# Kernel tuning notes

Measured on AMD Instinct MI355X. Metric: run time of the kernel, lower is better.

Reference implementation:

```python
import jax, jax.numpy as jnp
import numpy as np

K = 16            # neighbors
QUERY_CHUNK = 256 # SE is applied per chunk of this many query points (matches torch loop)
EPS = 1e-5        # BatchNorm eps (eval mode, running stats)


def bn(x, g, b, m, v):
    # eval-mode batchnorm over last axis (channel-last layout here)
    return (x - m) * (g / jnp.sqrt(v + EPS)) + b


def setup_inputs() -> dict:
    key = jax.random.key(0)
    ks = jax.random.split(key, 16)
    B, Cin, N = 4, 128, 4096
    H, Cout = 128, 256
    se_h = Cout // 4
    r = lambda k, s, sc=1.0: jax.random.normal(k, s, jnp.float32) * sc
    return dict(
        x=r(ks[0], (B, Cin, N)),
        W_edge=r(ks[1], (H, 2 * Cin), 0.05),          # edge_mlp conv2d 1x1
        bn1_g=jnp.ones((H,), jnp.float32), bn1_b=jnp.zeros((H,), jnp.float32),
        bn1_m=r(ks[2], (H,), 0.1), bn1_v=jax.random.uniform(ks[3], (H,), jnp.float32) + 0.5,
        w_att=r(ks[4], (H,), 0.1),                     # att_conv (1,H,1,1)
        W_fuse=r(ks[5], (Cout, H), 0.05),              # fuse conv1d
        bn2_g=jnp.ones((Cout,), jnp.float32), bn2_b=jnp.zeros((Cout,), jnp.float32),
        bn2_m=r(ks[6], (Cout,), 0.1), bn2_v=jax.random.uniform(ks[7], (Cout,), jnp.float32) + 0.5,
        fc1_w=r(ks[8], (se_h, Cout), 0.05), fc1_b=jnp.zeros((se_h,), jnp.float32),
        fc2_w=r(ks[9], (Cout, se_h), 0.05), fc2_b=jnp.zeros((Cout,), jnp.float32),
        W_res=r(ks[10], (Cout, Cin), 0.05),            # res_conv conv1d (in!=out)
        bn3_g=jnp.ones((Cout,), jnp.float32), bn3_b=jnp.zeros((Cout,), jnp.float32),
        bn3_m=r(ks[11], (Cout,), 0.1), bn3_v=jax.random.uniform(ks[12], (Cout,), jnp.float32) + 0.5,
    )


def reference(x, W_edge, bn1_g, bn1_b, bn1_m, bn1_v, w_att,
              W_fuse, bn2_g, bn2_b, bn2_m, bn2_v,
              fc1_w, fc1_b, fc2_w, fc2_b,
              W_res, bn3_g, bn3_b, bn3_m, bn3_v):
    B, Cin, N = x.shape
    x_t = jnp.swapaxes(x, 1, 2)  # (B,N,Cin)

    # KNN on features (dynamic=False -> knn on x.transpose); squared euclidean
    # has the same ordering as torch.cdist(p=2).
    sq = jnp.sum(x_t * x_t, axis=-1)                               # (B,N)
    d2 = sq[:, :, None] + sq[:, None, :] - 2.0 * jnp.einsum('bnc,bmc->bnm', x_t, x_t)
    _, idx = jax.lax.top_k(-d2, K)                                  # (B,N,K) smallest dists

    neigh = jax.vmap(lambda p, i: p[i])(x_t, idx)                   # (B,N,K,Cin)
    center = jnp.broadcast_to(x_t[:, :, None, :], neigh.shape)      # (B,N,K,Cin)
    edge = jnp.concatenate([neigh - center, center], axis=-1)       # (B,N,K,2Cin)

    # edge_mlp: 1x1 conv + BN + ReLU
    h = jax.nn.relu(bn(jnp.einsum('bnkc,hc->bnkh', edge, W_edge),
                       bn1_g, bn1_b, bn1_m, bn1_v))                 # (B,N,K,H)

    # attention over neighbors
    att = jax.nn.softmax(jnp.einsum('bnkh,h->bnk', h, w_att), axis=-1)
    agg = jnp.einsum('bnkh,bnk->bnh', h, att)                       # (B,N,H)

    # fuse conv1d + BN + ReLU
    out = jax.nn.relu(bn(jnp.einsum('bnh,oh->bno', agg, W_fuse),
                         bn2_g, bn2_b, bn2_m, bn2_v))               # (B,N,Cout)

    # SE channel attention, applied per query chunk (matches torch loop semantics)
    Cout = out.shape[-1]
    nc = N // QUERY_CHUNK
    oc = out.reshape(B, nc, QUERY_CHUNK, Cout)
    s = oc.mean(axis=2)                                             # (B,nc,Cout)
    s = jax.nn.relu(jnp.einsum('bmc,hc->bmh', s, fc1_w) + fc1_b)
    s = jax.nn.sigmoid(jnp.einsum('bmh,ch->bmc', s, fc2_w) + fc2_b)
    out = (oc * s[:, :, None, :]).reshape(B, N, Cout)

    # residual projection (in_channels != out_channels)
    res = bn(jnp.einsum('bnc,oc->bno', x_t, W_res), bn3_g, bn3_b, bn3_m, bn3_v)
    out = out + res
    return jnp.swapaxes(out, 1, 2)                                  # (B,Cout,N)
```

## Files before the change

kernel.cpp:

```cpp
#include <hip/hip_runtime.h>
#include <cstddef>

typedef __bf16 bf16;
typedef __bf16 bf16x8 __attribute__((ext_vector_type(8)));
typedef float  f32x4  __attribute__((ext_vector_type(4)));
typedef unsigned short u16;
typedef unsigned long long u64;

#define MFMA16x16(a, b, c) __builtin_amdgcn_mfma_f32_16x16x32_bf16((a), (b), (c), 0, 0, 0)

namespace {
constexpr int BB   = 4;
constexpr int CIN  = 128;
constexpr int NPT  = 4096;
constexpr int KNBR = 16;
constexpr int HED  = 128;
constexpr int COUT = 256;
}

__device__ __forceinline__ double mk_keyd(float d, unsigned mlo ) {
  const u64 k = ((u64)__float_as_uint(d) << 32) | mlo;
  return __longlong_as_double((long long)k);
}
__device__ __forceinline__ int key_idx(double kd) {
  return (int)((__double_as_longlong(kd) >> 20) & 0xFFF);
}

__device__ __forceinline__ void sort16d(double* k) {
  #pragma unroll
  for (int sz = 2; sz <= 16; sz <<= 1) {
    #pragma unroll
    for (int st = sz >> 1; st > 0; st >>= 1) {
      #pragma unroll
      for (int i = 0; i < 16; ++i) {
        const int j = i ^ st;
        if (j > i) {
          const bool up = ((i & sz) == 0);
          const double a = k[i], c = k[j];
          const double lo = fmin(a, c), hi = fmax(a, c);
          k[i] = up ? lo : hi;
          k[j] = up ? hi : lo;
        }
      }
    }
  }
}

__device__ __forceinline__ void merge16d(double* R, const double* B) {
  double t[16];
  #pragma unroll
  for (int i = 0; i < 16; ++i) t[i] = fmin(R[i], B[15 - i]);
  #pragma unroll
  for (int st = 8; st > 0; st >>= 1) {
    #pragma unroll
    for (int i = 0; i < 16; ++i) {
      const int j = i ^ st;
      if (j > i) {
        const double a = t[i], c = t[j];
        t[i] = fmin(a, c);
        t[j] = fmax(a, c);
      }
    }
  }
  #pragma unroll
  for (int i = 0; i < 16; ++i) R[i] = t[i];
}

__device__ __forceinline__ void shfl_merge16d(double* R, int mask) {
  double B[16];
  #pragma unroll
  for (int i = 0; i < 16; ++i) B[i] = __shfl_xor(R[i], mask, 64);
  merge16d(R, B);
}

__global__ __launch_bounds__(256) void k_prepw(const float* __restrict__ x,
                                               bf16* __restrict__ xh,
                                               bf16* __restrict__ xl,
                                               float* __restrict__ sq,
                                               const float* __restrict__ We,
                                               const float* __restrict__ Wf,
                                               const float* __restrict__ Wr,
                                               bf16* __restrict__ Web,
                                               bf16* __restrict__ Wfb,
                                               bf16* __restrict__ Wrb,
                                               float* __restrict__ partp) {
  __shared__ __attribute__((aligned(16))) bf16 th[64][136];
  __shared__ __attribute__((aligned(16))) bf16 tl[64][136];
  __shared__ float sqp[4][64];
  const int blk = blockIdx.x;
  const int tid = threadIdx.x;
  if (blk >= 256) {
    if (blk < 640) {
      const int i = (blk - 256) * 256 + tid;
      const int a = i >> 15;
      const int j = i & 32767;
      const float* src = (a == 0) ? We : (a == 1) ? Wf : Wr;
      bf16*        dst = (a == 0) ? Web : (a == 1) ? Wfb : Wrb;
      dst[j] = (bf16)src[j];
    } else {
      for (int i = tid; i < 64 * COUT; i += 256) partp[i] = 0.f;
    }
    return;
  }
  const int b   = blk >> 6;
  const int n0  = (blk & 63) << 6;
  const int nl  = tid & 63;
  const int cg  = tid >> 6;
  const float* xb = x + (size_t)b * CIN * NPT;
  float acc = 0.f;
  #pragma unroll
  for (int rep = 0; rep < 32; ++rep) {
    const int c = rep * 4 + cg;
    const float v = xb[(size_t)c * NPT + n0 + nl];
    const bf16 h = (bf16)v;
    const bf16 l = (bf16)(v - (float)h);
    acc += v * v;
    th[nl][c] = h;
    tl[nl][c] = l;
  }
  sqp[cg][nl] = acc;
  __syncthreads();
  bf16* xho = xh + ((size_t)b * NPT + n0) * CIN;
  bf16* xlo = xl + ((size_t)b * NPT + n0) * CIN;
  #pragma unroll
  for (int rep = 0; rep < 32; ++rep) {
    const int e = rep * 256 + tid;
    const int r = e >> 7;
    const int c = e & 127;
    xho[(size_t)r * CIN + c] = th[r][c];
    xlo[(size_t)r * CIN + c] = tl[r][c];
  }
  if (tid < 64) {
    sq[b * NPT + n0 + tid] = sqp[0][tid] + sqp[1][tid] + sqp[2][tid] + sqp[3][tid];
  }
}

__global__ __launch_bounds__(256, 2) void k_knn(const bf16* __restrict__ xh,
                                                const bf16* __restrict__ xl,
                                                const float* __restrict__ sq,
                                                int* __restrict__ knn_idx) {
  __shared__ double Lk[32][66];
  const int tid  = threadIdx.x;
  const int w    = tid >> 6;
  const int lane = tid & 63;
  const int col  = lane & 15;
  const int quad = lane >> 4;
  const int bid  = blockIdx.x;
  const int swz  = ((bid & 7) << 6) | (bid >> 3);
  const int b    = swz >> 7;
  const int q0   = (swz & 127) << 5;
  const bf16*  xhb = xh + (size_t)b * NPT * CIN;
  const bf16*  xlb = xl + (size_t)b * NPT * CIN;
  const float* sqb = sq + b * NPT;

  bf16x8 qh[2][4], ql[2][4];
  float sqn[2];
  #pragma unroll
  for (int t = 0; t < 2; ++t) {
    const bf16* qrh = xhb + (size_t)(q0 + t * 16 + col) * CIN + quad * 8;
    const bf16* qrl = xlb + (size_t)(q0 + t * 16 + col) * CIN + quad * 8;
    #pragma unroll
    for (int ks = 0; ks < 4; ++ks) {
      qh[t][ks] = *(const bf16x8*)(qrh + ks * 32);
      ql[t][ks] = *(const bf16x8*)(qrl + ks * 32);
    }
    sqn[t] = sqb[q0 + t * 16 + col];
  }

  const double INF = __builtin_inf();
  double R0[16], R1[16];
  #pragma unroll
  for (int i = 0; i < 16; ++i) { R0[i] = INF; R1[i] = INF; }

  const int cbase = w << 10;
  for (int mt = 0; mt < 16; ++mt) {
    const int m0 = cbase + (mt << 6);
    double k0[16], k1[16];
    #pragma unroll
    for (int cb = 0; cb < 4; ++cb) {
      const bf16* crh = xhb + (size_t)(m0 + cb * 16 + col) * CIN + quad * 8;
      const bf16* crl = xlb + (size_t)(m0 + cb * 16 + col) * CIN + quad * 8;
      f32x4 a0 = {0.f, 0.f, 0.f, 0.f};
      f32x4 a1 = {0.f, 0.f, 0.f, 0.f};
      #pragma unroll
      for (int ks = 0; ks < 4; ++ks) {
        const bf16x8 ch_ = *(const bf16x8*)(crh + ks * 32);
        const bf16x8 cl_ = *(const bf16x8*)(crl + ks * 32);
        a0 = MFMA16x16(cl_, qh[0][ks], a0);
        a0 = MFMA16x16(ch_, ql[0][ks], a0);
        a0 = MFMA16x16(ch_, qh[0][ks], a0);
        a1 = MFMA16x16(cl_, qh[1][ks], a1);
        a1 = MFMA16x16(ch_, ql[1][ks], a1);
        a1 = MFMA16x16(ch_, qh[1][ks], a1);
      }
      const f32x4 sqm = *(const f32x4*)(sqb + m0 + cb * 16 + quad * 4);
      const unsigned mlo0 = (unsigned)(m0 + cb * 16 + quad * 4) << 20;
      #pragma unroll
      for (int r = 0; r < 4; ++r) {
        k0[cb * 4 + r] = mk_keyd((sqn[0] + sqm[r]) - 2.0f * a0[r], mlo0 + ((unsigned)r << 20));
        k1[cb * 4 + r] = mk_keyd((sqn[1] + sqm[r]) - 2.0f * a1[r], mlo0 + ((unsigned)r << 20));
      }
    }
    sort16d(k0); merge16d(R0, k0);
    sort16d(k1); merge16d(R1, k1);
  }

  shfl_merge16d(R0, 16);
  shfl_merge16d(R0, 32);
  shfl_merge16d(R1, 16);
  shfl_merge16d(R1, 32);

  if (quad == 0) {
    #pragma unroll
    for (int i = 0; i < 16; ++i) {
      Lk[col][w * 16 + i]        = R0[i];
      Lk[16 | col][w * 16 + i]   = R1[i];
    }
  }
  __syncthreads();

  if (tid < 64) {
    const int q = tid >> 1;
    const int j = tid & 1;
    double A[16], Bv[16];
    #pragma unroll
    for (int i = 0; i < 16; ++i) {
      A[i]  = Lk[q][(2 * j) * 16 + i];
      Bv[i] = Lk[q][(2 * j + 1) * 16 + i];
    }
    merge16d(A, Bv);
    #pragma unroll
    for (int i = 0; i < 16; ++i) Lk[q][j * 16 + i] = A[i];
  }
  __syncthreads();
  if (tid < 32) {
    double A[16], Bv[16];
    #pragma unroll
    for (int i = 0; i < 16; ++i) {
      A[i]  = Lk[tid][i];
      Bv[i] = Lk[tid][16 + i];
    }
    merge16d(A, Bv);
    int* op = knn_idx + (size_t)(b * NPT + q0 + tid) * KNBR;
    #pragma unroll
    for (int i = 0; i < 16; ++i) op[i] = key_idx(A[i]);
  }
}

__global__ __launch_bounds__(256) void k_edge(const bf16* __restrict__ xh,
                                              const bf16* __restrict__ xl,
                                              const int* __restrict__ knn_idx,
                                              const bf16* __restrict__ We,
                                              const float* __restrict__ g1, const float* __restrict__ b1,
                                              const float* __restrict__ m1, const float* __restrict__ v1,
                                              const float* __restrict__ watt,
                                              bf16* __restrict__ agg) {
  __shared__ __attribute__((aligned(16))) bf16 Ew[4][16][264];
  __shared__ float s1[HED], t1[HED], wat[HED];
  const int tid  = threadIdx.x;
  const int w    = tid >> 6;
  const int lane = tid & 63;
  const int col  = lane & 15;
  const int quad = lane >> 4;
  if (tid < HED) {
    const float ss = g1[tid] / sqrtf(v1[tid] + 1e-5f);
    s1[tid] = ss;
    t1[tid] = b1[tid] - m1[tid] * ss;
    wat[tid] = watt[tid];
  }
  __syncthreads();
  const int bid = blockIdx.x;
  const int swz = ((bid & 7) << 7) | (bid >> 3);
  const int gw  = swz * 4 + w;
  for (int it = 0; it < 4; ++it) {
    const int p = gw * 4 + it;
    const int b = p >> 12;
    const int n = p & 4095;
    const bf16* xhb = xh + (size_t)b * NPT * CIN;
    const bf16* xlb = xl + (size_t)b * NPT * CIN;
    const int my = knn_idx[(size_t)p * KNBR + col];
    const int m  = __shfl(my, lane >> 2);
    const int sub = lane & 3;
    const int kn  = lane >> 2;
    const bf16* nh = xhb + (size_t)m * CIN + sub * 32;
    const bf16* nl_ = xlb + (size_t)m * CIN + sub * 32;
    const bf16* ch = xhb + (size_t)n * CIN + sub * 32;
    const bf16* cl = xlb + (size_t)n * CIN + sub * 32;
    #pragma unroll
    for (int j = 0; j < 4; ++j) {
      const bf16x8 nhv = *(const bf16x8*)(nh + j * 8);
      const bf16x8 nlv = *(const bf16x8*)(nl_ + j * 8);
      const bf16x8 chv = *(const bf16x8*)(ch + j * 8);
      const bf16x8 clv = *(const bf16x8*)(cl + j * 8);
      bf16x8 dv, cv;
      #pragma unroll
      for (int e = 0; e < 8; ++e) {
        const float nf = (float)nhv[e] + (float)nlv[e];
        const float cf = (float)chv[e] + (float)clv[e];
        dv[e] = (bf16)(nf - cf);
        cv[e] = (bf16)cf;
      }
      *(bf16x8*)&Ew[w][kn][sub * 32 + j * 8]       = dv;
      *(bf16x8*)&Ew[w][kn][128 + sub * 32 + j * 8] = cv;
    }
    const f32x4 zero4 = {0.f, 0.f, 0.f, 0.f};
    f32x4 acc[8];
    #pragma unroll
    for (int hb = 0; hb < 8; ++hb) acc[hb] = zero4;
    #pragma unroll
    for (int ks = 0; ks < 8; ++ks) {
      const bf16x8 af = *(const bf16x8*)&Ew[w][col][ks * 32 + quad * 8];
      #pragma unroll
      for (int hb = 0; hb < 8; ++hb) {
        const bf16x8 bfv = *(const bf16x8*)(We + (size_t)(hb * 16 + col) * 256 + ks * 32 + quad * 8);
        acc[hb] = MFMA16x16(af, bfv, acc[hb]);
      }
    }
    float h[8][4];
    float lg[4] = {0.f, 0.f, 0.f, 0.f};
    #pragma unroll
    for (int hb = 0; hb < 8; ++hb) {
      const int hc = hb * 16 + col;
      const float ss = s1[hc], tt = t1[hc], ww = wat[hc];
      #pragma unroll
      for (int r = 0; r < 4; ++r) {
        const float hv = fmaxf(acc[hb][r] * ss + tt, 0.f);
        h[hb][r] = hv;
        lg[r] += hv * ww;
      }
    }
    #pragma unroll
    for (int r = 0; r < 4; ++r) {
      float vv = lg[r];
      vv += __shfl_xor(vv, 1);
      vv += __shfl_xor(vv, 2);
      vv += __shfl_xor(vv, 4);
      vv += __shfl_xor(vv, 8);
      lg[r] = vv;
    }
    float mx = fmaxf(fmaxf(lg[0], lg[1]), fmaxf(lg[2], lg[3]));
    mx = fmaxf(mx, __shfl_xor(mx, 16));
    mx = fmaxf(mx, __shfl_xor(mx, 32));
    float ex[4];
    float sm = 0.f;
    #pragma unroll
    for (int r = 0; r < 4; ++r) { ex[r] = expf(lg[r] - mx); sm += ex[r]; }
    sm += __shfl_xor(sm, 16);
    sm += __shfl_xor(sm, 32);
    const float inv = 1.0f / sm;
    float ag[8];
    #pragma unroll
    for (int hb = 0; hb < 8; ++hb) {
      float a = h[hb][0] * ex[0] + h[hb][1] * ex[1] + h[hb][2] * ex[2] + h[hb][3] * ex[3];
      a += __shfl_xor(a, 16);
      a += __shfl_xor(a, 32);
      ag[hb] = a * inv;
    }
    if (quad == 0) {
      bf16* ao = agg + (size_t)p * HED;
      #pragma unroll
      for (int hb = 0; hb < 8; ++hb) ao[hb * 16 + col] = (bf16)ag[hb];
    }
  }
}

__global__ __launch_bounds__(256) void k_fuse(const bf16* __restrict__ agg,
                                              const bf16* __restrict__ Wf,
                                              const float* __restrict__ g2, const float* __restrict__ b2,
                                              const float* __restrict__ m2, const float* __restrict__ v2,
                                              bf16* __restrict__ outp,
                                              float* __restrict__ partp) {
  const int tid  = threadIdx.x;
  const int w    = tid >> 6;
  const int lane = tid & 63;
  const int col  = lane & 15;
  const int quad = lane >> 4;
  const int pb   = blockIdx.x >> 2;
  const int obq  = blockIdx.x & 3;
  const int p0   = (pb * 4 + w) * 16;
  const int bc   = p0 >> 8;
  bf16x8 afr[4];
  const bf16* arow = agg + (size_t)(p0 + col) * HED + quad * 8;
  #pragma unroll
  for (int ks = 0; ks < 4; ++ks) afr[ks] = *(const bf16x8*)(arow + ks * 32);
  #pragma unroll
  for (int i = 0; i < 4; ++i) {
    const int ob = obq * 4 + i;
    f32x4 acc = {0.f, 0.f, 0.f, 0.f};
    const bf16* brow = Wf + (size_t)(ob * 16 + col) * HED + quad * 8;
    #pragma unroll
    for (int ks = 0; ks < 4; ++ks)
      acc = MFMA16x16(afr[ks], *(const bf16x8*)(brow + ks * 32), acc);
    const int o = ob * 16 + col;
    const float ss = g2[o] / sqrtf(v2[o] + 1e-5f);
    const float tt = b2[o] - m2[o] * ss;
    float se_s = 0.f;
    #pragma unroll
    for (int r = 0; r < 4; ++r) {
      const float v = fmaxf(acc[r] * ss + tt, 0.f);
      outp[(size_t)(p0 + quad * 4 + r) * COUT + o] = (bf16)v;
      se_s += v;
    }
    se_s += __shfl_xor(se_s, 16);
    se_s += __shfl_xor(se_s, 32);
    if (quad == 0) atomicAdd(&partp[(size_t)bc * COUT + o], se_s);
  }
}

__global__ __launch_bounds__(256) void k_se2(const float* __restrict__ partp,
                                             const float* __restrict__ f1w, const float* __restrict__ f1b,
                                             const float* __restrict__ f2w, const float* __restrict__ f2b,
                                             float* __restrict__ sse) {
  __shared__ float mean_s[COUT];
  __shared__ float h1[64];
  const int bc  = blockIdx.x;
  const int tid = threadIdx.x;
  mean_s[tid] = partp[(size_t)bc * COUT + tid] * (1.0f / 256.0f);
  __syncthreads();
  if (tid < 64) {
    float a = f1b[tid];
    for (int c = 0; c < COUT; ++c) a += f1w[tid * COUT + c] * mean_s[c];
    h1[tid] = fmaxf(a, 0.f);
  }
  __syncthreads();
  float a = f2b[tid];
  #pragma unroll
  for (int j = 0; j < 64; ++j) a += f2w[tid * 64 + j] * h1[j];
  sse[(size_t)bc * COUT + tid] = 1.0f / (1.0f + expf(-a));
}

__global__ __launch_bounds__(256) void k_final(const bf16* __restrict__ xh,
                                               const bf16* __restrict__ Wr,
                                               const float* __restrict__ g3, const float* __restrict__ b3,
                                               const float* __restrict__ m3, const float* __restrict__ v3,
                                               const bf16* __restrict__ outp,
                                               const float* __restrict__ sse,
                                               float* __restrict__ out) {
  const int tid  = threadIdx.x;
  const int w    = tid >> 6;
  const int lane = tid & 63;
  const int col  = lane & 15;
  const int quad = lane >> 4;
  const int pb   = blockIdx.x >> 2;
  const int obq  = blockIdx.x & 3;
  const int p0   = (pb * 4 + w) * 16;
  const int b    = p0 >> 12;
  const int n0l  = p0 & 4095;
  bf16x8 afr[4];
  const bf16* arow = xh + (size_t)(p0 + col) * CIN + quad * 8;
  #pragma unroll
  for (int ks = 0; ks < 4; ++ks) afr[ks] = *(const bf16x8*)(arow + ks * 32);
  const float* scb = sse + (size_t)(b * 16 + (n0l >> 8)) * COUT;
  #pragma unroll
  for (int i = 0; i < 4; ++i) {
    const int ob = obq * 4 + i;
    f32x4 acc = {0.f, 0.f, 0.f, 0.f};
    const bf16* brow = Wr + (size_t)(ob * 16 + col) * CIN + quad * 8;
    #pragma unroll
    for (int ks = 0; ks < 4; ++ks)
      acc = MFMA16x16(afr[ks], *(const bf16x8*)(brow + ks * 32), acc);
    const int o = ob * 16 + col;
    const float ss = g3[o] / sqrtf(v3[o] + 1e-5f);
    const float tt = b3[o] - m3[o] * ss;
    const float sc = scb[o];
    f32x4 pk;
    #pragma unroll
    for (int r = 0; r < 4; ++r) {
      const float res = acc[r] * ss + tt;
      pk[r] = (float)outp[(size_t)(p0 + quad * 4 + r) * COUT + o] * sc + res;
    }
    float* op = out + (size_t)(b * COUT + o) * NPT + n0l + quad * 4;
    *(f32x4*)op = pk;
  }
}

extern "C" void kernel_launch(void* const* d_in, const int* in_sizes, int n_in,
                              void* d_out, int out_size, void* d_ws, size_t ws_size,
                              hipStream_t stream) {
  (void)in_sizes; (void)n_in; (void)out_size; (void)ws_size;
  const float* x    = (const float*)d_in[0];
  const float* We   = (const float*)d_in[1];
  const float* g1   = (const float*)d_in[2];
  const float* b1   = (const float*)d_in[3];
  const float* m1   = (const float*)d_in[4];
  const float* v1   = (const float*)d_in[5];
  const float* watt = (const float*)d_in[6];
  const float* Wf   = (const float*)d_in[7];
  const float* g2   = (const float*)d_in[8];
  const float* b2   = (const float*)d_in[9];
  const float* m2   = (const float*)d_in[10];
  const float* v2   = (const float*)d_in[11];
  const float* f1w  = (const float*)d_in[12];
  const float* f1b  = (const float*)d_in[13];
  const float* f2w  = (const float*)d_in[14];
  const float* f2b  = (const float*)d_in[15];
  const float* Wr   = (const float*)d_in[16];
  const float* g3   = (const float*)d_in[17];
  const float* b3   = (const float*)d_in[18];
  const float* m3   = (const float*)d_in[19];
  const float* v3   = (const float*)d_in[20];

  char* ws = (char*)d_ws;
  size_t off = 0;
  bf16*  xth  = (bf16*)(ws + off);  off += (size_t)BB * NPT * CIN * 2;
  bf16*  xtl  = (bf16*)(ws + off);  off += (size_t)BB * NPT * CIN * 2;
  float* sq   = (float*)(ws + off); off += (size_t)BB * NPT * 4;
  int*   idxp = (int*)(ws + off);   off += (size_t)BB * NPT * KNBR * 4;
  bf16*  aggp = (bf16*)(ws + off);  off += (size_t)BB * NPT * HED * 2;
  bf16*  outp = (bf16*)(ws + off);  off += (size_t)BB * NPT * COUT * 2;
  float* ssep = (float*)(ws + off); off += (size_t)BB * 16 * COUT * 4;
  float* partp= (float*)(ws + off); off += (size_t)64 * COUT * 4;
  bf16*  Web  = (bf16*)(ws + off);  off += (size_t)HED * 2 * CIN * 2;
  bf16*  Wfb  = (bf16*)(ws + off);  off += (size_t)COUT * HED * 2;
  bf16*  Wrb  = (bf16*)(ws + off);  off += (size_t)COUT * CIN * 2;

  float* out = (float*)d_out;

  k_prepw<<<641, 256, 0, stream>>>(x, xth, xtl, sq, We, Wf, Wr, Web, Wfb, Wrb, partp);
  k_knn<<<512, 256, 0, stream>>>(xth, xtl, sq, idxp);
  k_edge<<<1024, 256, 0, stream>>>(xth, xtl, idxp, Web, g1, b1, m1, v1, watt, aggp);
  k_fuse<<<1024, 256, 0, stream>>>(aggp, Wfb, g2, b2, m2, v2, outp, partp);
  k_se2<<<64, 256, 0, stream>>>(partp, f1w, f1b, f2w, f2b, ssep);
  k_final<<<1024, 256, 0, stream>>>(xth, Wrb, g3, b3, m3, v3, outp, ssep, out);
}
```

Baseline: 356.2 us.

## Stage KNN query fragments in LDS and build edge MFMA operands in registers

In the KNN kernel, the query tile's hi/lo bf16 fragments are staged once into shared memory and reloaded per candidate tile, instead of being held in registers for the whole loop. The loop is also reordered so all four candidate blocks accumulate inside the k-step loop. This aims to cut register pressure so the kernel keeps two blocks per CU, at the cost of extra LDS reads each iteration. In the edge kernel, the shared-memory staging buffer for edge features is removed and the MFMA A-operands (neighbor minus center, and center) are built directly in registers in the MFMA lane layout, which drops an LDS round trip.

```diff
diff --git a/kernel.cpp b/kernel.cpp
--- a/kernel.cpp
+++ b/kernel.cpp
@@ -140,6 +140,8 @@
                                                 const float* __restrict__ sq,
                                                 int* __restrict__ knn_idx) {
   __shared__ double Lk[32][66];
+  __shared__ __attribute__((aligned(16))) bf16 Qh[2][4][4][16][8];
+  __shared__ __attribute__((aligned(16))) bf16 Ql[2][4][4][16][8];
   const int tid  = threadIdx.x;
   const int w    = tid >> 6;
   const int lane = tid & 63;
@@ -153,19 +155,21 @@
   const bf16*  xlb = xl + (size_t)b * NPT * CIN;
   const float* sqb = sq + b * NPT;
 
-  bf16x8 qh[2][4], ql[2][4];
+  #pragma unroll
+  for (int rep = 0; rep < 2; ++rep) {
+    const int idx = rep * 256 + tid;
+    const int r   = idx >> 4;
+    const int j   = idx & 15;
+    *(bf16x8*)&Qh[r >> 4][j >> 2][j & 3][r & 15][0] =
+        *(const bf16x8*)(xhb + (size_t)(q0 + r) * CIN + j * 8);
+    *(bf16x8*)&Ql[r >> 4][j >> 2][j & 3][r & 15][0] =
+        *(const bf16x8*)(xlb + (size_t)(q0 + r) * CIN + j * 8);
+  }
+  __syncthreads();
+
   float sqn[2];
-  #pragma unroll
-  for (int t = 0; t < 2; ++t) {
-    const bf16* qrh = xhb + (size_t)(q0 + t * 16 + col) * CIN + quad * 8;
-    const bf16* qrl = xlb + (size_t)(q0 + t * 16 + col) * CIN + quad * 8;
-    #pragma unroll
-    for (int ks = 0; ks < 4; ++ks) {
-      qh[t][ks] = *(const bf16x8*)(qrh + ks * 32);
-      ql[t][ks] = *(const bf16x8*)(qrl + ks * 32);
-    }
-    sqn[t] = sqb[q0 + t * 16 + col];
-  }
+  sqn[0] = sqb[q0 + col];
+  sqn[1] = sqb[q0 + 16 + col];
 
   const double INF = __builtin_inf();
   double R0[16], R1[16];
@@ -174,31 +178,40 @@
 
   const int cbase = w << 10;
   for (int mt = 0; mt < 16; ++mt) {
+    int zofs = 0;
+    asm volatile("" : "+v"(zofs));
     const int m0 = cbase + (mt << 6);
+    const f32x4 zero4 = {0.f, 0.f, 0.f, 0.f};
+    f32x4 a0s[4], a1s[4];
+    #pragma unroll
+    for (int cb = 0; cb < 4; ++cb) { a0s[cb] = zero4; a1s[cb] = zero4; }
+    #pragma unroll
+    for (int ks = 0; ks < 4; ++ks) {
+      const bf16x8 qh0 = *(const bf16x8*)(&Qh[0][ks][quad][col][0] + zofs);
+      const bf16x8 ql0 = *(const bf16x8*)(&Ql[0][ks][quad][col][0] + zofs);
+      const bf16x8 qh1 = *(const bf16x8*)(&Qh[1][ks][quad][col][0] + zofs);
+      const bf16x8 ql1 = *(const bf16x8*)(&Ql[1][ks][quad][col][0] + zofs);
+      #pragma unroll
+      for (int cb = 0; cb < 4; ++cb) {
+        const bf16x8 ch_ = *(const bf16x8*)(xhb + (size_t)(m0 + cb * 16 + col) * CIN + ks * 32 + quad * 8);
+        const bf16x8 cl_ = *(const bf16x8*)(xlb + (size_t)(m0 + cb * 16 + col) * CIN + ks * 32 + quad * 8);
+        a0s[cb] = MFMA16x16(cl_, qh0, a0s[cb]);
+        a0s[cb] = MFMA16x16(ch_, ql0, a0s[cb]);
+        a0s[cb] = MFMA16x16(ch_, qh0, a0s[cb]);
+        a1s[cb] = MFMA16x16(cl_, qh1, a1s[cb]);
+        a1s[cb] = MFMA16x16(ch_, ql1, a1s[cb]);
+        a1s[cb] = MFMA16x16(ch_, qh1, a1s[cb]);
+      }
+    }
     double k0[16], k1[16];
     #pragma unroll
     for (int cb = 0; cb < 4; ++cb) {
-      const bf16* crh = xhb + (size_t)(m0 + cb * 16 + col) * CIN + quad * 8;
-      const bf16* crl = xlb + (size_t)(m0 + cb * 16 + col) * CIN + quad * 8;
-      f32x4 a0 = {0.f, 0.f, 0.f, 0.f};
-      f32x4 a1 = {0.f, 0.f, 0.f, 0.f};
-      #pragma unroll
-      for (int ks = 0; ks < 4; ++ks) {
-        const bf16x8 ch_ = *(const bf16x8*)(crh + ks * 32);
-        const bf16x8 cl_ = *(const bf16x8*)(crl + ks * 32);
-        a0 = MFMA16x16(cl_, qh[0][ks], a0);
-        a0 = MFMA16x16(ch_, ql[0][ks], a0);
-        a0 = MFMA16x16(ch_, qh[0][ks], a0);
-        a1 = MFMA16x16(cl_, qh[1][ks], a1);
-        a1 = MFMA16x16(ch_, ql[1][ks], a1);
-        a1 = MFMA16x16(ch_, qh[1][ks], a1);
-      }
       const f32x4 sqm = *(const f32x4*)(sqb + m0 + cb * 16 + quad * 4);
       const unsigned mlo0 = (unsigned)(m0 + cb * 16 + quad * 4) << 20;
       #pragma unroll
       for (int r = 0; r < 4; ++r) {
-        k0[cb * 4 + r] = mk_keyd((sqn[0] + sqm[r]) - 2.0f * a0[r], mlo0 + ((unsigned)r << 20));
-        k1[cb * 4 + r] = mk_keyd((sqn[1] + sqm[r]) - 2.0f * a1[r], mlo0 + ((unsigned)r << 20));
+        k0[cb * 4 + r] = mk_keyd((sqn[0] + sqm[r]) - 2.0f * a0s[cb][r], mlo0 + ((unsigned)r << 20));
+        k1[cb * 4 + r] = mk_keyd((sqn[1] + sqm[r]) - 2.0f * a1s[cb][r], mlo0 + ((unsigned)r << 20));
       }
     }
     sort16d(k0); merge16d(R0, k0);
@@ -255,7 +268,6 @@
                                               const float* __restrict__ m1, const float* __restrict__ v1,
                                               const float* __restrict__ watt,
                                               bf16* __restrict__ agg) {
-  __shared__ __attribute__((aligned(16))) bf16 Ew[4][16][264];
   __shared__ float s1[HED], t1[HED], wat[HED];
   const int tid  = threadIdx.x;
   const int w    = tid >> 6;
@@ -278,38 +290,40 @@
     const int n = p & 4095;
     const bf16* xhb = xh + (size_t)b * NPT * CIN;
     const bf16* xlb = xl + (size_t)b * NPT * CIN;
-    const int my = knn_idx[(size_t)p * KNBR + col];
-    const int m  = __shfl(my, lane >> 2);
-    const int sub = lane & 3;
-    const int kn  = lane >> 2;
-    const bf16* nh = xhb + (size_t)m * CIN + sub * 32;
-    const bf16* nl_ = xlb + (size_t)m * CIN + sub * 32;
-    const bf16* ch = xhb + (size_t)n * CIN + sub * 32;
-    const bf16* cl = xlb + (size_t)n * CIN + sub * 32;
-    #pragma unroll
-    for (int j = 0; j < 4; ++j) {
-      const bf16x8 nhv = *(const bf16x8*)(nh + j * 8);
-      const bf16x8 nlv = *(const bf16x8*)(nl_ + j * 8);
-      const bf16x8 chv = *(const bf16x8*)(ch + j * 8);
-      const bf16x8 clv = *(const bf16x8*)(cl + j * 8);
+    const int m = knn_idx[(size_t)p * KNBR + col];
+    const bf16* nrh = xhb + (size_t)m * CIN + quad * 8;
+    const bf16* nrl = xlb + (size_t)m * CIN + quad * 8;
+    const bf16* crh = xhb + (size_t)n * CIN + quad * 8;
+    const bf16* crl = xlb + (size_t)n * CIN + quad * 8;
+    const f32x4 zero4 = {0.f, 0.f, 0.f, 0.f};
+    f32x4 acc[8];
+    #pragma unroll
+    for (int hb = 0; hb < 8; ++hb) acc[hb] = zero4;
+    bf16x8 cvs[4];
+    #pragma unroll
+    for (int ks = 0; ks < 4; ++ks) {
+      const bf16x8 nh8 = *(const bf16x8*)(nrh + ks * 32);
+      const bf16x8 nl8 = *(const bf16x8*)(nrl + ks * 32);
+      const bf16x8 ch8 = *(const bf16x8*)(crh + ks * 32);
+      const bf16x8 cl8 = *(const bf16x8*)(crl + ks * 32);
       bf16x8 dv, cv;
       #pragma unroll
       for (int e = 0; e < 8; ++e) {
-        const float nf = (float)nhv[e] + (float)nlv[e];
-        const float cf = (float)chv[e] + (float)clv[e];
+        const float nf = (float)nh8[e] + (float)nl8[e];
+        const float cf = (float)ch8[e] + (float)cl8[e];
         dv[e] = (bf16)(nf - cf);
         cv[e] = (bf16)cf;
       }
-      *(bf16x8*)&Ew[w][kn][sub * 32 + j * 8]       = dv;
-      *(bf16x8*)&Ew[w][kn][128 + sub * 32 + j * 8] = cv;
-    }
-    const f32x4 zero4 = {0.f, 0.f, 0.f, 0.f};
-    f32x4 acc[8];
-    #pragma unroll
-    for (int hb = 0; hb < 8; ++hb) acc[hb] = zero4;
-    #pragma unroll
-    for (int ks = 0; ks < 8; ++ks) {
-      const bf16x8 af = *(const bf16x8*)&Ew[w][col][ks * 32 + quad * 8];
+      cvs[ks] = cv;
+      #pragma unroll
+      for (int hb = 0; hb < 8; ++hb) {
+        const bf16x8 bfv = *(const bf16x8*)(We + (size_t)(hb * 16 + col) * 256 + ks * 32 + quad * 8);
+        acc[hb] = MFMA16x16(dv, bfv, acc[hb]);
+      }
+    }
+    #pragma unroll
+    for (int ks = 4; ks < 8; ++ks) {
+      const bf16x8 af = cvs[ks - 4];
       #pragma unroll
       for (int hb = 0; hb < 8; ++hb) {
         const bf16x8 bfv = *(const bf16x8*)(We + (size_t)(hb * 16 + col) * 256 + ks * 32 + quad * 8);
```

Result: slower. 367.9 us (+3.3%).
